# Kernel tuning notes

Hardware: AMD Instinct MI355X
Metric: run time of the kernel (lower is better)

Reference implementation:

```python
import jax, jax.numpy as jnp
import numpy as np

N_NODES = 100_000
N_EDGES = 1_600_000
D_FEAT = 128
D_HID = 128
D_OUT = 1


def _w(key, fan_in, fan_out):
    # PyG Linear default (glorot-ish); exact init irrelevant for a math reference
    return jax.random.normal(key, (fan_in, fan_out), dtype=jnp.float32) * (1.0 / np.sqrt(fan_in))


def setup_inputs() -> dict:
    key = jax.random.key(0)
    ks = jax.random.split(key, 20)
    inp = {
        "x": jax.random.normal(ks[0], (N_NODES, D_FEAT), dtype=jnp.float32),
        "edge_index": jax.random.randint(ks[1], (2, N_EDGES), 0, N_NODES, dtype=jnp.int32),
    }
    dims = [(D_FEAT, D_HID), (D_HID, D_HID), (D_HID, D_OUT)]
    i = 2
    for li, (din, dout) in enumerate(dims, start=1):
        inp[f"Wk{li}"] = _w(ks[i + 0], din, dout)
        inp[f"Wq{li}"] = _w(ks[i + 1], din, dout)
        inp[f"Wv{li}"] = _w(ks[i + 2], din, dout)
        inp[f"Ws{li}"] = _w(ks[i + 3], din, dout)
        inp[f"b{li}"] = jnp.zeros((dout,), dtype=jnp.float32)
        i += 4
    return inp


def _res_gated_conv(x, src, dst, Wk, Wq, Wv, Ws, b):
    # out_i = Ws x_i + b + sum_{j->i} sigmoid(Wk x_i + Wq x_j) * (Wv x_j)
    k = x @ Wk          # [N, Dout] (keyed by target)
    q = x @ Wq          # [N, Dout] (keyed by source)
    v = x @ Wv          # [N, Dout]
    eta = jax.nn.sigmoid(k[dst] + q[src])          # [E, Dout] edge gate
    msg = eta * v[src]                             # [E, Dout]
    agg = jax.ops.segment_sum(msg, dst, num_segments=x.shape[0])  # scatter-add
    return agg + x @ Ws + b


def reference(x, edge_index, Wk1, Wq1, Wv1, Ws1, b1, Wk2, Wq2, Wv2, Ws2, b2,
              Wk3, Wq3, Wv3, Ws3, b3):
    src = edge_index[0]
    dst = edge_index[1]
    x = jax.nn.relu(_res_gated_conv(x, src, dst, Wk1, Wq1, Wv1, Ws1, b1))
    x = jax.nn.relu(_res_gated_conv(x, src, dst, Wk2, Wq2, Wv2, Ws2, b2))
    return _res_gated_conv(x, src, dst, Wk3, Wq3, Wv3, Ws3, b3)  # [N, 1]
```

## Files before the change

### kernel.cpp

```cpp
#include <hip/hip_runtime.h>
#include <hip/hip_bf16.h>
#include <cstdint>

typedef unsigned short u16;
typedef unsigned int   u32;
typedef __attribute__((ext_vector_type(8))) short bf16x8;
typedef __attribute__((ext_vector_type(4))) float f32x4;

#define NEG_LOG2E -1.44269504088896f

__device__ __forceinline__ float bf2f(u16 u) {
    union { u32 i; float f; } c; c.i = ((u32)u) << 16; return c.f;
}
__device__ __forceinline__ u16 f2bf(float f) {
    union { float f; u32 i; } c; c.f = f;
    u32 x = c.i;
    return (u16)((x + 0x7fffu + ((x >> 16) & 1u)) >> 16);
}
__device__ __forceinline__ void bfu2(u32 p, float& lo, float& hi) {
    union { u32 i; float f; } a, b;
    a.i = p << 16; b.i = p & 0xffff0000u;
    lo = a.f; hi = b.f;
}
__device__ __forceinline__ float gate(float zt) {
    return __builtin_amdgcn_rcpf(1.0f + __builtin_amdgcn_exp2f(zt));
}

#define CSR_CH 2048
#define XS 136

struct P8 { const float* p[8]; };
__global__ __launch_bounds__(256)
void prep_hist_k(P8 wsrc, u16* __restrict__ Wt,
                 const int* __restrict__ dst, int* __restrict__ cnt,
                 int nE, int NA, int nbuck) {
    __shared__ int lh[512];
    int t = threadIdx.x;
    if (blockIdx.x < 64) {
        int mat = blockIdx.x >> 3, seg = blockIdx.x & 7;
        const float* W = wsrc.p[mat];
        u16* T = Wt + (size_t)mat * 16384;
        for (int p = 0; p < 8; ++p) {
            int idx = seg * 2048 + p * 256 + t;
            int k = idx >> 7, n = idx & 127;
            T[n * 128 + k] = f2bf(W[k * 128 + n]);
        }
    } else {
        int b = blockIdx.x - 64;
        for (int i = t; i < nbuck; i += 256) lh[i] = 0;
        __syncthreads();
        int i0 = b * CSR_CH, iend = min(i0 + CSR_CH, nE);
        for (int i = i0 + t; i < iend; i += 256) atomicAdd(&lh[dst[i] >> 8], 1);
        __syncthreads();
        for (int i = t; i < nbuck; i += 256) cnt[i * NA + b] = lh[i];
    }
}

__global__ __launch_bounds__(256)
void scan_part_k(const int* __restrict__ arr, int* __restrict__ part, int M) {
    __shared__ int wsum[4];
    int t = threadIdx.x, lane = t & 63, wave = t >> 6;
    int i0 = blockIdx.x * 1024 + t * 4;
    int s = 0;
    for (int j = 0; j < 4; ++j) { int i = i0 + j; if (i < M) s += arr[i]; }
    for (int off = 32; off > 0; off >>= 1) s += __shfl_xor(s, off);
    if (lane == 0) wsum[wave] = s;
    __syncthreads();
    if (t == 0) part[blockIdx.x] = wsum[0] + wsum[1] + wsum[2] + wsum[3];
}

__global__ __launch_bounds__(256)
void scan_emit2_k(const int* __restrict__ arr, const int* __restrict__ part,
                  int* __restrict__ outp, int M, int total, int nparts) {
    __shared__ int sh[512];
    __shared__ int woff[4];
    int t = threadIdx.x, lane = t & 63, wave = t >> 6;
    sh[t]       = (t < nparts)       ? part[t]       : 0;
    sh[t + 256] = (t + 256 < nparts) ? part[t + 256] : 0;
    __syncthreads();
    for (int off = 1; off < 512; off <<= 1) {
        int u0 = (t >= off)       ? sh[t - off]       : 0;
        int u1 = (t + 256 >= off) ? sh[t + 256 - off] : 0;
        __syncthreads();
        sh[t] += u0; sh[t + 256] += u1;
        __syncthreads();
    }
    int base = (blockIdx.x == 0) ? 0 : sh[blockIdx.x - 1];
    __syncthreads();

    int i0 = blockIdx.x * 1024 + t * 4;
    int d[4]; int s = 0;
    for (int j = 0; j < 4; ++j) { int i = i0 + j; d[j] = (i < M) ? arr[i] : 0; s += d[j]; }
    int ws = s;
    for (int off = 1; off < 64; off <<= 1) {
        int u = __shfl_up(ws, off);
        if (lane >= off) ws += u;
    }
    if (lane == 63) woff[wave] = ws;
    __syncthreads();
    for (int w = 0; w < wave; ++w) base += woff[w];
    int ex = base + ws - s;
    for (int j = 0; j < 4; ++j) {
        int i = i0 + j;
        if (i < M) outp[i] = ex;
        ex += d[j];
    }
    if (blockIdx.x == 0 && t == 0) outp[M] = total;
}

__global__ __launch_bounds__(256)
void sortA_scat(const int* __restrict__ src, const int* __restrict__ dst,
                const int* __restrict__ scnt, u32* __restrict__ tkey,
                int nE, int NA, int nbuck) {
    __shared__ int lh[512];
    __shared__ int lbase[512];
    int t = threadIdx.x, b = blockIdx.x;
    for (int i = t; i < nbuck; i += 256) { lh[i] = 0; lbase[i] = scnt[i * NA + b]; }
    __syncthreads();
    int i0 = b * CSR_CH, iend = min(i0 + CSR_CH, nE);
    for (int i = i0 + t; i < iend; i += 256) {
        int d = dst[i], s = src[i];
        int bk = d >> 8;
        int r = atomicAdd(&lh[bk], 1);
        tkey[lbase[bk] + r] = ((u32)(d & 255) << 24) | (u32)s;
    }
}

__device__ __forceinline__
void sortB_body(const u32* __restrict__ tkey, const int* __restrict__ scnt,
                int* __restrict__ rowp, int* __restrict__ ssrc,
                int NA, int N, int nE, int b, int* h, int* offv) {
    int t = threadIdx.x;
    int base = scnt[b * NA];
    int endp = scnt[(b + 1) * NA];
    h[t] = 0;
    __syncthreads();
    for (int i = base + t; i < endp; i += 256)
        atomicAdd(&h[tkey[i] >> 24], 1);
    __syncthreads();
    int v = h[t];
    offv[t] = v;
    __syncthreads();
    for (int d = 1; d < 256; d <<= 1) {
        int u = (t >= d) ? offv[t - d] : 0;
        __syncthreads();
        offv[t] += u;
        __syncthreads();
    }
    int ex = offv[t] - v;
    __syncthreads();
    offv[t] = ex;
    h[t] = 0;
    __syncthreads();
    int dglob = b * 256 + t;
    if (dglob < N) rowp[dglob] = base + ex;
    if (b == 0 && t == 0) rowp[N] = nE;
    for (int i = base + t; i < endp; i += 256) {
        u32 k = tkey[i];
        int loc = k >> 24;
        int r = atomicAdd(&h[loc], 1);
        ssrc[base + offv[loc] + r] = (int)(k & 0xFFFFFFu);
    }
}

template<int F32>
__device__ __forceinline__
void gemm_body(int bid, u16* xs,
               const void* __restrict__ Xv, const u16* __restrict__ Wt,
               const float* __restrict__ bias,
               u16* __restrict__ KS, u16* __restrict__ QV, int nrows)
{
    const int tid  = threadIdx.x;
    const int wave = tid >> 6, lane = tid & 63;
    const int quad = lane >> 4, l16 = lane & 15;
    const int r0 = bid * 128;

    for (int p = 0; p < 8; ++p) {
        int c = p * 256 + tid;
        int row = c >> 4;
        int col = (c & 15) * 8;
        int gr = r0 + row; if (gr >= nrows) gr = nrows - 1;
        if (F32) {
            const float* sp = (const float*)Xv + (size_t)gr * 128 + col;
            float4 f0 = *(const float4*)(sp);
            float4 f1 = *(const float4*)(sp + 4);
            uint4 st;
            st.x = ((u32)f2bf(f0.y) << 16) | f2bf(f0.x);
            st.y = ((u32)f2bf(f0.w) << 16) | f2bf(f0.z);
            st.z = ((u32)f2bf(f1.y) << 16) | f2bf(f1.x);
            st.w = ((u32)f2bf(f1.w) << 16) | f2bf(f1.z);
            *(uint4*)(&xs[row * XS + col]) = st;
        } else {
            uint4 d = *(const uint4*)((const u16*)Xv + (size_t)gr * 128 + col);
            *(uint4*)(&xs[row * XS + col]) = d;
        }
    }
    __syncthreads();

    const int cbase = wave * 32;

    for (int pass = 0; pass < 2; ++pass) {
        const u16* WA = Wt + (size_t)(pass ? 0 : 1) * 16384;
        const u16* WB = Wt + (size_t)(pass ? 3 : 2) * 16384;

        bf16x8 afA0[4], afA1[4], afB0[4], afB1[4];
        for (int kt = 0; kt < 4; ++kt) {
            const int ro0 = (cbase + l16)      * 128 + kt * 32 + quad * 8;
            const int ro1 = (cbase + 16 + l16) * 128 + kt * 32 + quad * 8;
            afA0[kt] = *(const bf16x8*)(WA + ro0);
            afA1[kt] = *(const bf16x8*)(WA + ro1);
            afB0[kt] = *(const bf16x8*)(WB + ro0);
            afB1[kt] = *(const bf16x8*)(WB + ro1);
        }

        float4 bias4[2];
        if (pass) {
            bias4[0] = *(const float4*)(bias + cbase + quad * 4);
            bias4[1] = *(const float4*)(bias + cbase + 16 + quad * 4);
        }

        for (int nt = 0; nt < 8; ++nt) {
            f32x4 aA0 = (f32x4)0.0f, aA1 = (f32x4)0.0f;
            f32x4 aB0 = (f32x4)0.0f, aB1 = (f32x4)0.0f;
            for (int kt = 0; kt < 4; ++kt) {
                bf16x8 b = *(const bf16x8*)&xs[(nt * 16 + l16) * XS + kt * 32 + quad * 8];
                aA0 = __builtin_amdgcn_mfma_f32_16x16x32_bf16(afA0[kt], b, aA0, 0, 0, 0);
                aA1 = __builtin_amdgcn_mfma_f32_16x16x32_bf16(afA1[kt], b, aA1, 0, 0, 0);
                aB0 = __builtin_amdgcn_mfma_f32_16x16x32_bf16(afB0[kt], b, aB0, 0, 0, 0);
                aB1 = __builtin_amdgcn_mfma_f32_16x16x32_bf16(afB1[kt], b, aB1, 0, 0, 0);
            }
            int node = r0 + nt * 16 + l16;
            if (node >= nrows) continue;
            u16* rowbase = (pass ? KS : QV) + (size_t)node * 256;
            {
                float x0 = aA0[0] * NEG_LOG2E, x1 = aA0[1] * NEG_LOG2E;
                float x2 = aA0[2] * NEG_LOG2E, x3 = aA0[3] * NEG_LOG2E;
                float y0 = aB0[0], y1 = aB0[1], y2 = aB0[2], y3 = aB0[3];
                if (pass) { y0 += bias4[0].x; y1 += bias4[0].y; y2 += bias4[0].z; y3 += bias4[0].w; }
                uint4 out;
                out.x = ((u32)f2bf(x1) << 16) | f2bf(x0);
                out.y = ((u32)f2bf(x3) << 16) | f2bf(x2);
                out.z = ((u32)f2bf(y1) << 16) | f2bf(y0);
                out.w = ((u32)f2bf(y3) << 16) | f2bf(y2);
                *(uint4*)(rowbase + 2 * (cbase + quad * 4)) = out;
            }
            {
                float x0 = aA1[0] * NEG_LOG2E, x1 = aA1[1] * NEG_LOG2E;
                float x2 = aA1[2] * NEG_LOG2E, x3 = aA1[3] * NEG_LOG2E;
                float y0 = aB1[0], y1 = aB1[1], y2 = aB1[2], y3 = aB1[3];
                if (pass) { y0 += bias4[1].x; y1 += bias4[1].y; y2 += bias4[1].z; y3 += bias4[1].w; }
                uint4 out;
                out.x = ((u32)f2bf(x1) << 16) | f2bf(x0);
                out.y = ((u32)f2bf(x3) << 16) | f2bf(x2);
                out.z = ((u32)f2bf(y1) << 16) | f2bf(y0);
                out.w = ((u32)f2bf(y3) << 16) | f2bf(y2);
                *(uint4*)(rowbase + 2 * (cbase + 16 + quad * 4)) = out;
            }
        }
    }
}

__global__ __launch_bounds__(256, 2)
void sortB_gemm1(const u32* __restrict__ tkey, const int* __restrict__ scnt,
                 int* __restrict__ rowp, int* __restrict__ ssrc,
                 int NA, int N, int nE, int nbuck,
                 const float* __restrict__ x0, const u16* __restrict__ Wt,
                 const float* __restrict__ bias,
                 u16* __restrict__ KS, u16* __restrict__ QV)
{
    __shared__ u16 xs[128 * XS];
    if ((int)blockIdx.x < nbuck) {
        int* h = (int*)xs;
        int* offv = h + 256;
        sortB_body(tkey, scnt, rowp, ssrc, NA, N, nE, blockIdx.x, h, offv);
    } else {
        gemm_body<1>(blockIdx.x - nbuck, xs, x0, Wt, bias, KS, QV, N);
    }
}

__global__ __launch_bounds__(256, 2)
void gemm_l2(const u16* __restrict__ X, const u16* __restrict__ Wt,
             const float* __restrict__ bias,
             u16* __restrict__ KS, u16* __restrict__ QV, int nrows)
{
    __shared__ u16 xs[128 * XS];
    gemm_body<0>(blockIdx.x, xs, X, Wt, bias, KS, QV, nrows);
}

template<int MODE>
__global__ __launch_bounds__(256)
void edge_csr2(const int* __restrict__ rowp, const int* __restrict__ ssrc,
               const u16* __restrict__ KS, const u16* __restrict__ QV,
               u16* __restrict__ Xout,
               const float* __restrict__ Wk3, const float* __restrict__ Wq3,
               const float* __restrict__ Wv3, const float* __restrict__ Ws3,
               const float* __restrict__ b3,
               float* __restrict__ k3, float2* __restrict__ qv3,
               float* __restrict__ s3, int N)
{
    const int lane = threadIdx.x & 63;
    const int half = lane >> 5;
    const int t    = lane & 31;
    int gw = blockIdx.x * (blockDim.x >> 6) + (threadIdx.x >> 6);
    int nw = gridDim.x * (blockDim.x >> 6);

    float4 wk4, wq4, wv4, ws4;
    float bias3 = 0.0f;
    if (MODE == 1) {
        wk4 = *(const float4*)(Wk3 + 4 * t);
        wq4 = *(const float4*)(Wq3 + 4 * t);
        wv4 = *(const float4*)(Wv3 + 4 * t);
        ws4 = *(const float4*)(Ws3 + 4 * t);
        bias3 = b3[0];
    }

#define LOAD2(S0, S1) (*((const uint4*)(QV + (size_t)(half ? (S1) : (S0)) * 256) + t))
#define COMP(QVv, A0, A1, A2, A3)                                             \
    {                                                                         \
        float q0_, q1_, q2_, q3_, v0_, v1_, v2_, v3_;                         \
        bfu2((QVv).x, q0_, q1_); bfu2((QVv).y, q2_, q3_);                     \
        bfu2((QVv).z, v0_, v1_); bfu2((QVv).w, v2_, v3_);                     \
        A0 += gate(k0 + q0_) * v0_;  A1 += gate(k1 + q1_) * v1_;              \
        A2 += gate(k2 + q2_) * v2_;  A3 += gate(k3v + q3_) * v3_;             \
    }
#define LOADG(SVV, G, RA, RB)                                                 \
    {                                                                         \
        int s0_ = __builtin_amdgcn_readlane(SVV, 4 * (G));                    \
        int s1_ = __builtin_amdgcn_readlane(SVV, 4 * (G) + 1);                \
        int s2_ = __builtin_amdgcn_readlane(SVV, 4 * (G) + 2);                \
        int s3_ = __builtin_amdgcn_readlane(SVV, 4 * (G) + 3);                \
        RA = LOAD2(s0_, s1_); RB = LOAD2(s2_, s3_);                           \
    }

    int d = gw;
    int beg = 0, end = 0, sv = 0;
    uint4 ks; ks.x = ks.y = ks.z = ks.w = 0u;
    if (d < N) {
        beg = rowp[d]; end = rowp[d + 1];
        int e  = beg + lane;
        int ec = (end > beg) ? ((e < end) ? e : end - 1) : 0;
        sv = ssrc[ec];
        ks = *((const uint4*)KS + (size_t)d * 32 + t);
    }
    int havePF = 0;
    uint4 pA, pB;
    pA.x = pA.y = pA.z = pA.w = 0u;
    pB = pA;

    while (d < N) {
        int dn = d + nw;
        int begN = 0, endN = 0, svN = 0;
        uint4 ksN; ksN.x = ksN.y = ksN.z = ksN.w = 0u;
        if (dn < N) {
            begN = rowp[dn]; endN = rowp[dn + 1];
            int e  = begN + lane;
            int ec = (endN > begN) ? ((e < endN) ? e : endN - 1) : 0;
            svN = ssrc[ec];
            ksN = *((const uint4*)KS + (size_t)dn * 32 + t);
        }

        float k0, k1, k2, k3v;
        bfu2(ks.x, k0, k1); bfu2(ks.y, k2, k3v);
        float a0 = 0.f, a1 = 0.f, a2 = 0.f, a3 = 0.f;
        float e0 = 0.f, e1 = 0.f, e2 = 0.f, e3 = 0.f;

        for (int base = beg; base < end; base += 64) {
            if (base > beg) {
                int e  = base + lane;
                int ec = (e < end) ? e : end - 1;
                sv = ssrc[ec];
            }
            int m = end - base; if (m > 64) m = 64;
            int ng = m >> 2;
            int j = ng << 2;
            if (ng > 0) {
                uint4 xA, xB, yA, yB;
                if (havePF && base == beg) { xA = pA; xB = pB; }
                else LOADG(sv, 0, xA, xB);
                int g = 1;
                for (; g + 1 < ng; g += 2) {
                    LOADG(sv, g, yA, yB);
                    COMP(xA, a0, a1, a2, a3);
                    COMP(xB, e0, e1, e2, e3);
                    LOADG(sv, g + 1, xA, xB);
                    COMP(yA, a0, a1, a2, a3);
                    COMP(yB, e0, e1, e2, e3);
                }
                if (g < ng) {
                    LOADG(sv, g, yA, yB);
                    COMP(xA, a0, a1, a2, a3);
                    COMP(xB, e0, e1, e2, e3);
                    COMP(yA, a0, a1, a2, a3);
                    COMP(yB, e0, e1, e2, e3);
                } else {
                    COMP(xA, a0, a1, a2, a3);
                    COMP(xB, e0, e1, e2, e3);
                }
            }
            if (j + 2 <= m) {
                int s0 = __builtin_amdgcn_readlane(sv, j);
                int s1 = __builtin_amdgcn_readlane(sv, j + 1);
                uint4 qA = LOAD2(s0, s1);
                COMP(qA, a0, a1, a2, a3);
                j += 2;
            }
            if (j < m) {
                int s0i = __builtin_amdgcn_readlane(sv, j);
                uint4 qv_ = *((const uint4*)(QV + (size_t)s0i * 256) + t);
                float q0_, q1_, q2_, q3_, v0_, v1_, v2_, v3_;
                bfu2(qv_.x, q0_, q1_); bfu2(qv_.y, q2_, q3_);
                bfu2(qv_.z, v0_, v1_); bfu2(qv_.w, v2_, v3_);
                if (half == 0) {
                    a0 += gate(k0 + q0_) * v0_;  a1 += gate(k1 + q1_) * v1_;
                    a2 += gate(k2 + q2_) * v2_;  a3 += gate(k3v + q3_) * v3_;
                }
            }
        }

        havePF = 0;
        if (dn < N) {
            int mN = endN - begN; if (mN > 64) mN = 64;
            if ((mN >> 2) > 0) {
                int s0_ = __builtin_amdgcn_readlane(svN, 0);
                int s1_ = __builtin_amdgcn_readlane(svN, 1);
                int s2_ = __builtin_amdgcn_readlane(svN, 2);
                int s3_ = __builtin_amdgcn_readlane(svN, 3);
                pA = LOAD2(s0_, s1_);
                pB = LOAD2(s2_, s3_);
                havePF = 1;
            }
        }
#undef LOADG
#undef LOAD2
#undef COMP

        a0 += e0; a1 += e1; a2 += e2; a3 += e3;
        a0 += __shfl_xor(a0, 32);
        a1 += __shfl_xor(a1, 32);
        a2 += __shfl_xor(a2, 32);
        a3 += __shfl_xor(a3, 32);

        float s0f, s1f, s2f, s3f;
        bfu2(ks.z, s0f, s1f); bfu2(ks.w, s2f, s3f);
        float r0 = fmaxf(s0f + a0, 0.f);
        float r1 = fmaxf(s1f + a1, 0.f);
        float r2 = fmaxf(s2f + a2, 0.f);
        float r3 = fmaxf(s3f + a3, 0.f);

        if (MODE == 0) {
            if (half == 0) {
                uint2 st;
                st.x = ((u32)f2bf(r1) << 16) | f2bf(r0);
                st.y = ((u32)f2bf(r3) << 16) | f2bf(r2);
                *(uint2*)(Xout + (size_t)d * 128 + t * 4) = st;
            }
        } else {
            float pk = r0 * wk4.x + r1 * wk4.y + r2 * wk4.z + r3 * wk4.w;
            float pq = r0 * wq4.x + r1 * wq4.y + r2 * wq4.z + r3 * wq4.w;
            float pv = r0 * wv4.x + r1 * wv4.y + r2 * wv4.z + r3 * wv4.w;
            float ps = r0 * ws4.x + r1 * ws4.y + r2 * ws4.z + r3 * ws4.w;
            for (int off = 1; off < 32; off <<= 1) {
                pk += __shfl_xor(pk, off);
                pq += __shfl_xor(pq, off);
                pv += __shfl_xor(pv, off);
                ps += __shfl_xor(ps, off);
            }
            if (lane == 0) {
                k3[d]  = NEG_LOG2E * pk;
                qv3[d] = make_float2(NEG_LOG2E * pq, pv);
                s3[d]  = ps + bias3;
            }
        }

        d = dn; beg = begN; end = endN; sv = svN; ks = ksN;
    }
}

__global__ __launch_bounds__(256)
void edge3_csr(const int* __restrict__ rowp, const int* __restrict__ ssrc,
               const float* __restrict__ k3, const float2* __restrict__ qv3,
               const float* __restrict__ s3, float* __restrict__ outp, int N)
{
    int lane = threadIdx.x & 63;
    int gw = blockIdx.x * (blockDim.x >> 6) + (threadIdx.x >> 6);
    int nw = gridDim.x * (blockDim.x >> 6);

    int d = gw;
    int beg = 0, end = 0, sv = 0;
    float kd = 0.f, sd = 0.f;
    if (d < N) {
        beg = rowp[d]; end = rowp[d + 1];
        int e  = beg + lane;
        int ec = (end > beg) ? ((e < end) ? e : end - 1) : 0;
        sv = ssrc[ec];
        kd = k3[d]; sd = s3[d];
    }
    while (d < N) {
        int dn = d + nw;
        int begN = 0, endN = 0, svN = 0;
        float kdN = 0.f, sdN = 0.f;
        if (dn < N) {
            begN = rowp[dn]; endN = rowp[dn + 1];
            int e  = begN + lane;
            int ec = (endN > begN) ? ((e < endN) ? e : endN - 1) : 0;
            svN = ssrc[ec];
            kdN = k3[dn]; sdN = s3[dn];
        }

        float sum = 0.0f;
        int m = end - beg;
        if (lane < m) {
            float2 qv = qv3[sv];
            sum = gate(kd + qv.x) * qv.y;
        }
        for (int e = beg + 64 + lane; e < end; e += 64) {
            float2 qv = qv3[ssrc[e]];
            sum += gate(kd + qv.x) * qv.y;
        }
        for (int off = 32; off > 0; off >>= 1) sum += __shfl_xor(sum, off);
        if (lane == 0) outp[d] = sd + sum;

        d = dn; beg = begN; end = endN; sv = svN; kd = kdN; sd = sdN;
    }
}

extern "C" void kernel_launch(void* const* d_in, const int* in_sizes, int n_in,
                              void* d_out, int out_size, void* d_ws, size_t ws_size,
                              hipStream_t stream)
{
    const float* x0 = (const float*)d_in[0];
    const int*   ei = (const int*)d_in[1];
    const int    N  = in_sizes[0] / 128;
    const int    E  = in_sizes[1] / 2;
    const int* src = ei;
    const int* dst = ei + E;

    const int NBUCK = (N + 255) >> 8;
    const int NA    = (E + CSR_CH - 1) / CSR_CH;
    const int M     = NBUCK * NA;
    const int nparts = (M + 1023) / 1024;

    char* ws = (char*)d_ws;
    size_t off = 0;
    auto carve = [&](size_t bytes) { void* p = ws + off; off += (bytes + 255) & ~(size_t)255; return p; };
    u16*    Wt   = (u16*)carve((size_t)8 * 16384 * sizeof(u16));
    u16*    bufX = (u16*)carve((size_t)N * 128 * sizeof(u16));
    u16*    KS   = (u16*)carve((size_t)N * 256 * sizeof(u16));
    u16*    QV   = (u16*)carve((size_t)N * 256 * sizeof(u16));
    int*    ssrc = (int*)carve((size_t)E * sizeof(int));
    u32*    tkey = (u32*)carve((size_t)E * sizeof(u32));
    int*    rowp = (int*)carve((size_t)(N + 1) * sizeof(int));
    int*    cnt  = (int*)carve((size_t)M * sizeof(int));
    int*    scnt = (int*)carve((size_t)(M + 1) * sizeof(int));
    int*    part = (int*)carve((size_t)512 * sizeof(int));
    float*  k3   = (float*)carve((size_t)N * sizeof(float));
    float2* qv3  = (float2*)carve((size_t)N * sizeof(float2));
    float*  s3   = (float*)carve((size_t)N * sizeof(float));

    P8 wp;
    wp.p[0] = (const float*)d_in[2];  wp.p[1] = (const float*)d_in[3];
    wp.p[2] = (const float*)d_in[4];  wp.p[3] = (const float*)d_in[5];
    wp.p[4] = (const float*)d_in[7];  wp.p[5] = (const float*)d_in[8];
    wp.p[6] = (const float*)d_in[9];  wp.p[7] = (const float*)d_in[10];

    int gb = (N + 127) / 128;

    prep_hist_k<<<64 + NA, 256, 0, stream>>>(wp, Wt, dst, cnt, E, NA, NBUCK);
    scan_part_k<<<nparts, 256, 0, stream>>>(cnt, part, M);
    scan_emit2_k<<<nparts, 256, 0, stream>>>(cnt, part, scnt, M, E, nparts);
    sortA_scat<<<NA, 256, 0, stream>>>(src, dst, scnt, tkey, E, NA, NBUCK);
    sortB_gemm1<<<NBUCK + gb, 256, 0, stream>>>(tkey, scnt, rowp, ssrc, NA, N, E, NBUCK,
        x0, Wt, (const float*)d_in[6], KS, QV);
    edge_csr2<0><<<4096, 256, 0, stream>>>(rowp, ssrc, KS, QV, bufX,
        nullptr, nullptr, nullptr, nullptr, nullptr, nullptr, nullptr, nullptr, N);
    gemm_l2<<<gb, 256, 0, stream>>>(bufX, Wt + 4 * 16384, (const float*)d_in[11], KS, QV, N);
    edge_csr2<1><<<4096, 256, 0, stream>>>(rowp, ssrc, KS, QV, nullptr,
        (const float*)d_in[12], (const float*)d_in[13], (const float*)d_in[14],
        (const float*)d_in[15], (const float*)d_in[16],
        k3, qv3, s3, N);
    edge3_csr<<<2048, 256, 0, stream>>>(rowp, ssrc, k3, qv3, s3, (float*)d_out, N);
}
```

Baseline: 503.5 us.

## Replace bucketed two-pass CSR sort with global atomic counting sort

Builds the CSR by counting edges per destination node with global atomics, scanning the per-node counts into row pointers and a cursor array, then scattering sources via atomic cursor increments fused with the first GEMM. This removes the bucket histogram layout, the intermediate key array and the per-bucket local sort pass, and drops one kernel launch. In exchange it relies on global atomic throughput, adds a memset, and makes neighbor order within each row nondeterministic, which changes the floating-point summation order.

```diff
diff --git a/kernel.cpp b/kernel.cpp
--- a/kernel.cpp
+++ b/kernel.cpp
@@ -31,10 +31,8 @@
 
 struct P8 { const float* p[8]; };
 __global__ __launch_bounds__(256)
-void prep_hist_k(P8 wsrc, u16* __restrict__ Wt,
-                 const int* __restrict__ dst, int* __restrict__ cnt,
-                 int nE, int NA, int nbuck) {
-    __shared__ int lh[512];
+void prep_hist2_k(P8 wsrc, u16* __restrict__ Wt,
+                  const int* __restrict__ dst, int* __restrict__ cnt, int nE) {
     int t = threadIdx.x;
     if (blockIdx.x < 64) {
         int mat = blockIdx.x >> 3, seg = blockIdx.x & 7;
@@ -47,12 +45,9 @@
         }
     } else {
         int b = blockIdx.x - 64;
-        for (int i = t; i < nbuck; i += 256) lh[i] = 0;
-        __syncthreads();
         int i0 = b * CSR_CH, iend = min(i0 + CSR_CH, nE);
-        for (int i = i0 + t; i < iend; i += 256) atomicAdd(&lh[dst[i] >> 8], 1);
-        __syncthreads();
-        for (int i = t; i < nbuck; i += 256) cnt[i * NA + b] = lh[i];
+        for (int i = i0 + t; i < iend; i += 256)
+            atomicAdd(&cnt[dst[i]], 1);
     }
 }
 
@@ -71,7 +66,8 @@
 
 __global__ __launch_bounds__(256)
 void scan_emit2_k(const int* __restrict__ arr, const int* __restrict__ part,
-                  int* __restrict__ outp, int M, int total, int nparts) {
+                  int* __restrict__ outp, int* __restrict__ cur,
+                  int M, int total, int nparts) {
     __shared__ int sh[512];
     __shared__ int woff[4];
     int t = threadIdx.x, lane = t & 63, wave = t >> 6;
@@ -102,65 +98,10 @@
     int ex = base + ws - s;
     for (int j = 0; j < 4; ++j) {
         int i = i0 + j;
-        if (i < M) outp[i] = ex;
+        if (i < M) { outp[i] = ex; cur[i] = ex; }
         ex += d[j];
     }
     if (blockIdx.x == 0 && t == 0) outp[M] = total;
-}
-
-__global__ __launch_bounds__(256)
-void sortA_scat(const int* __restrict__ src, const int* __restrict__ dst,
-                const int* __restrict__ scnt, u32* __restrict__ tkey,
-                int nE, int NA, int nbuck) {
-    __shared__ int lh[512];
-    __shared__ int lbase[512];
-    int t = threadIdx.x, b = blockIdx.x;
-    for (int i = t; i < nbuck; i += 256) { lh[i] = 0; lbase[i] = scnt[i * NA + b]; }
-    __syncthreads();
-    int i0 = b * CSR_CH, iend = min(i0 + CSR_CH, nE);
-    for (int i = i0 + t; i < iend; i += 256) {
-        int d = dst[i], s = src[i];
-        int bk = d >> 8;
-        int r = atomicAdd(&lh[bk], 1);
-        tkey[lbase[bk] + r] = ((u32)(d & 255) << 24) | (u32)s;
-    }
-}
-
-__device__ __forceinline__
-void sortB_body(const u32* __restrict__ tkey, const int* __restrict__ scnt,
-                int* __restrict__ rowp, int* __restrict__ ssrc,
-                int NA, int N, int nE, int b, int* h, int* offv) {
-    int t = threadIdx.x;
-    int base = scnt[b * NA];
-    int endp = scnt[(b + 1) * NA];
-    h[t] = 0;
-    __syncthreads();
-    for (int i = base + t; i < endp; i += 256)
-        atomicAdd(&h[tkey[i] >> 24], 1);
-    __syncthreads();
-    int v = h[t];
-    offv[t] = v;
-    __syncthreads();
-    for (int d = 1; d < 256; d <<= 1) {
-        int u = (t >= d) ? offv[t - d] : 0;
-        __syncthreads();
-        offv[t] += u;
-        __syncthreads();
-    }
-    int ex = offv[t] - v;
-    __syncthreads();
-    offv[t] = ex;
-    h[t] = 0;
-    __syncthreads();
-    int dglob = b * 256 + t;
-    if (dglob < N) rowp[dglob] = base + ex;
-    if (b == 0 && t == 0) rowp[N] = nE;
-    for (int i = base + t; i < endp; i += 256) {
-        u32 k = tkey[i];
-        int loc = k >> 24;
-        int r = atomicAdd(&h[loc], 1);
-        ssrc[base + offv[loc] + r] = (int)(k & 0xFFFFFFu);
-    }
 }
 
 template<int F32>
@@ -261,20 +202,24 @@
 }
 
 __global__ __launch_bounds__(256, 2)
-void sortB_gemm1(const u32* __restrict__ tkey, const int* __restrict__ scnt,
-                 int* __restrict__ rowp, int* __restrict__ ssrc,
-                 int NA, int N, int nE, int nbuck,
-                 const float* __restrict__ x0, const u16* __restrict__ Wt,
-                 const float* __restrict__ bias,
-                 u16* __restrict__ KS, u16* __restrict__ QV)
+void scat_gemm1(const int* __restrict__ src, const int* __restrict__ dst,
+                int* __restrict__ cur, int* __restrict__ ssrc,
+                int nE, int gb,
+                const float* __restrict__ x0, const u16* __restrict__ Wt,
+                const float* __restrict__ bias,
+                u16* __restrict__ KS, u16* __restrict__ QV, int N)
 {
     __shared__ u16 xs[128 * XS];
-    if ((int)blockIdx.x < nbuck) {
-        int* h = (int*)xs;
-        int* offv = h + 256;
-        sortB_body(tkey, scnt, rowp, ssrc, NA, N, nE, blockIdx.x, h, offv);
+    if ((int)blockIdx.x < gb) {
+        gemm_body<1>(blockIdx.x, xs, x0, Wt, bias, KS, QV, N);
     } else {
-        gemm_body<1>(blockIdx.x - nbuck, xs, x0, Wt, bias, KS, QV, N);
+        int b = blockIdx.x - gb;
+        int i0 = b * CSR_CH, iend = min(i0 + CSR_CH, nE);
+        for (int i = i0 + threadIdx.x; i < iend; i += 256) {
+            int d = dst[i], s = src[i];
+            int r = atomicAdd(&cur[d], 1);
+            ssrc[r] = s;
+        }
     }
 }
 
@@ -535,10 +480,8 @@
     const int* src = ei;
     const int* dst = ei + E;
 
-    const int NBUCK = (N + 255) >> 8;
-    const int NA    = (E + CSR_CH - 1) / CSR_CH;
-    const int M     = NBUCK * NA;
-    const int nparts = (M + 1023) / 1024;
+    const int NA     = (E + CSR_CH - 1) / CSR_CH;
+    const int nparts = (N + 1023) / 1024;
 
     char* ws = (char*)d_ws;
     size_t off = 0;
@@ -548,10 +491,9 @@
     u16*    KS   = (u16*)carve((size_t)N * 256 * sizeof(u16));
     u16*    QV   = (u16*)carve((size_t)N * 256 * sizeof(u16));
     int*    ssrc = (int*)carve((size_t)E * sizeof(int));
-    u32*    tkey = (u32*)carve((size_t)E * sizeof(u32));
     int*    rowp = (int*)carve((size_t)(N + 1) * sizeof(int));
-    int*    cnt  = (int*)carve((size_t)M * sizeof(int));
-    int*    scnt = (int*)carve((size_t)(M + 1) * sizeof(int));
+    int*    cnt  = (int*)carve((size_t)N * sizeof(int));
+    int*    cur  = (int*)carve((size_t)N * sizeof(int));
     int*    part = (int*)carve((size_t)512 * sizeof(int));
     float*  k3   = (float*)carve((size_t)N * sizeof(float));
     float2* qv3  = (float2*)carve((size_t)N * sizeof(float2));
@@ -565,12 +507,12 @@
 
     int gb = (N + 127) / 128;
 
-    prep_hist_k<<<64 + NA, 256, 0, stream>>>(wp, Wt, dst, cnt, E, NA, NBUCK);
-    scan_part_k<<<nparts, 256, 0, stream>>>(cnt, part, M);
-    scan_emit2_k<<<nparts, 256, 0, stream>>>(cnt, part, scnt, M, E, nparts);
-    sortA_scat<<<NA, 256, 0, stream>>>(src, dst, scnt, tkey, E, NA, NBUCK);
-    sortB_gemm1<<<NBUCK + gb, 256, 0, stream>>>(tkey, scnt, rowp, ssrc, NA, N, E, NBUCK,
-        x0, Wt, (const float*)d_in[6], KS, QV);
+    hipMemsetAsync(cnt, 0, (size_t)N * sizeof(int), stream);
+    prep_hist2_k<<<64 + NA, 256, 0, stream>>>(wp, Wt, dst, cnt, E);
+    scan_part_k<<<nparts, 256, 0, stream>>>(cnt, part, N);
+    scan_emit2_k<<<nparts, 256, 0, stream>>>(cnt, part, rowp, cur, N, E, nparts);
+    scat_gemm1<<<gb + NA, 256, 0, stream>>>(src, dst, cur, ssrc, E, gb,
+        x0, Wt, (const float*)d_in[6], KS, QV, N);
     edge_csr2<0><<<4096, 256, 0, stream>>>(rowp, ssrc, KS, QV, bufX,
         nullptr, nullptr, nullptr, nullptr, nullptr, nullptr, nullptr, nullptr, N);
     gemm_l2<<<gb, 256, 0, stream>>>(bufX, Wt + 4 * 16384, (const float*)d_in[11], KS, QV, N);
```

After: 588.8 us. 1.17x slower.
